# Kernel tuning notes

Measured on AMD Instinct MI355X. Metric: run time of the kernel, lower is better.

Reference implementation:

```python
import jax, jax.numpy as jnp
import numpy as np

H = 1024; NH = 16; HD = H // NH  # hidden, heads, head_dim

def setup_inputs() -> dict:
    key = jax.random.key(0)
    ks = jax.random.split(key, 9)
    s = 1.0 / np.sqrt(H)
    return {
        "hidden_states": jax.random.normal(ks[0], (2, 2048, H), jnp.float32),
        "Wq": jax.random.uniform(ks[1], (H, H), jnp.float32, -s, s),
        "bq": jnp.zeros((H,), jnp.float32),
        "Wk": jax.random.uniform(ks[2], (H, H), jnp.float32, -s, s),
        "bk": jnp.zeros((H,), jnp.float32),
        "Wv": jax.random.uniform(ks[3], (H, H), jnp.float32, -s, s),
        "bv": jnp.zeros((H,), jnp.float32),
        "Wo": jax.random.uniform(ks[4], (H, H), jnp.float32, -s, s),
        "bo": jnp.zeros((H,), jnp.float32),
    }

def reference(hidden_states, Wq, bq, Wk, bk, Wv, bv, Wo, bo):
    B, S, _ = hidden_states.shape
    def heads(x):  # [B,S,H] -> [B,NH,S,HD]
        return x.reshape(B, S, NH, HD).transpose(0, 2, 1, 3)
    q = heads(hidden_states @ Wq + bq)
    k = heads(hidden_states @ Wk + bk)
    v = heads(hidden_states @ Wv + bv)
    scores = jnp.einsum('bhqd,bhkd->bhqk', q, k) / jnp.sqrt(jnp.float32(HD))
    causal = jnp.where(jnp.tril(jnp.ones((S, S), bool)), 0.0, -jnp.inf)
    probs = jax.nn.softmax(scores + causal[None, None], axis=-1)
    ctx = jnp.einsum('bhqk,bhkd->bhqd', probs, v)
    ctx = ctx.transpose(0, 2, 1, 3).reshape(B, S, H)
    return ctx @ Wo + bo
```

## Files before the change

### kernel.cpp

```cpp
#include <hip/hip_runtime.h>
#include <hip/hip_bf16.h>

#define BB 2
#define SS 2048
#define HH 1024
#define NHH 16
#define HDD 64
#define MM (BB*SS)
#define QKV_N (3*HH)

typedef _Float16 f16x8 __attribute__((ext_vector_type(8)));
typedef _Float16 f16x4 __attribute__((ext_vector_type(4)));
typedef float f32x4 __attribute__((ext_vector_type(4)));

#define MFMA16(a,b,c) __builtin_amdgcn_mfma_f32_16x16x32_f16((a),(b),(c),0,0,0)

__device__ __forceinline__ void gl2lds16(const _Float16* g, _Float16* l) {
    __builtin_amdgcn_global_load_lds(
        (const __attribute__((address_space(1))) void*)g,
        (__attribute__((address_space(3))) void*)l, 16, 0, 0);
}

__global__ void prep_kernel(const float* __restrict__ X,
                            const float* __restrict__ W0, const float* __restrict__ W1,
                            const float* __restrict__ W2, const float* __restrict__ W3,
                            _Float16* __restrict__ Xh,
                            _Float16* __restrict__ WqkvT, _Float16* __restrict__ WoT) {
    __shared__ float t[32][33];
    int z = blockIdx.z;
    int tx = threadIdx.x, ty = threadIdx.y;
    if (z >= 4) {
        size_t row0 = (size_t)(z - 4) * 1024 + blockIdx.y * 32;
        int col0 = blockIdx.x * 32;
#pragma unroll
        for (int r = ty; r < 32; r += 8) {
            float v = X[(row0 + r) * HH + col0 + tx];
            Xh[(row0 + r) * HH + col0 + tx] = (_Float16)v;
        }
        return;
    }
    const float* src = (z == 0) ? W0 : (z == 1) ? W1 : (z == 2) ? W2 : W3;
    _Float16* dst = (z < 3) ? (WqkvT + (size_t)z * HH * HH) : WoT;
    int k0 = blockIdx.y * 32, n0 = blockIdx.x * 32;
#pragma unroll
    for (int r = ty; r < 32; r += 8)
        t[r][tx] = src[(size_t)(k0 + r) * HH + (n0 + tx)];
    __syncthreads();
#pragma unroll
    for (int r = ty; r < 32; r += 8)
        dst[(size_t)(n0 + r) * HH + (k0 + tx)] = (_Float16)t[tx][r];
}

template<int MODE>
__global__ __launch_bounds__(256) void gemm128_kernel(
    const _Float16* __restrict__ A, const _Float16* __restrict__ Bt,
    const float* __restrict__ bias0, const float* __restrict__ bias1, const float* __restrict__ bias2,
    _Float16* __restrict__ Qh, _Float16* __restrict__ Kh, _Float16* __restrict__ Vt,
    float* __restrict__ Out)
{
    const int K = HH;
    const int NT = K / 32;
    __shared__ _Float16 smem[16896];

    int row0 = blockIdx.y * 128, n0 = blockIdx.x * 128;
    int tid = threadIdx.x;
    int w = tid >> 6, l = tid & 63, m16 = l & 15, quad = l >> 4;
    int wm = w >> 1, wn = w & 1;

    int srow = w * 32 + (l >> 2);
    int sch = (l & 3) ^ ((l >> 2) & 3) ^ ((l >> 4) & 3);
    const _Float16* aptr = A + (size_t)(row0 + srow) * K + sch * 8;
    const _Float16* bptr = Bt + (size_t)(n0 + srow) * K + sch * 8;

    int gsw = (m16 & 3) ^ ((m16 >> 2) & 3);
    int acol = (quad ^ gsw) * 8;

    f32x4 zero4 = {0.f, 0.f, 0.f, 0.f};
    f32x4 acc[4][4];
#pragma unroll
    for (int i = 0; i < 4; ++i)
#pragma unroll
        for (int j = 0; j < 4; ++j) acc[i][j] = zero4;

    auto stage = [&](int t, int buf) {
        int k0 = t * 32;
        int ao = buf * 4096 + (w * 32) * 32;
        int bo = 8192 + buf * 4096 + (w * 32) * 32;
        gl2lds16(aptr + k0, smem + ao);
        gl2lds16(aptr + (size_t)16 * K + k0, smem + ao + 16 * 32);
        gl2lds16(bptr + k0, smem + bo);
        gl2lds16(bptr + (size_t)16 * K + k0, smem + bo + 16 * 32);
    };

    stage(0, 0);
    for (int t = 0; t < NT; ++t) {
        int cur = t & 1;
        asm volatile("s_waitcnt vmcnt(0)" ::: "memory");
        __syncthreads();
        if (t + 1 < NT) stage(t + 1, cur ^ 1);
        const _Float16* Asr = smem + cur * 4096;
        const _Float16* Bsr = smem + 8192 + cur * 4096;
        f16x8 af[4], bf[4];
#pragma unroll
        for (int i = 0; i < 4; ++i)
            af[i] = *(const f16x8*)&Asr[(wm * 64 + i * 16 + m16) * 32 + acol];
#pragma unroll
        for (int j = 0; j < 4; ++j)
            bf[j] = *(const f16x8*)&Bsr[(wn * 64 + j * 16 + m16) * 32 + acol];
#pragma unroll
        for (int i = 0; i < 4; ++i)
#pragma unroll
            for (int j = 0; j < 4; ++j)
                acc[i][j] = MFMA16(af[i], bf[j], acc[i][j]);
    }

    if (MODE == 1) {
#pragma unroll
        for (int j = 0; j < 4; ++j) {
            int n = n0 + wn * 64 + j * 16 + m16;
            float bi = bias0[n];
#pragma unroll
            for (int i = 0; i < 4; ++i)
#pragma unroll
                for (int r = 0; r < 4; ++r) {
                    int mg = row0 + wm * 64 + i * 16 + quad * 4 + r;
                    Out[(size_t)mg * HH + n] = acc[i][j][r] + bi;
                }
        }
        return;
    }

    int which = n0 >> 10;
    const float* bias = (which == 0) ? bias0 : (which == 1) ? bias1 : bias2;
    __syncthreads();
#pragma unroll
    for (int j = 0; j < 4; ++j) {
        int n_local = wn * 64 + j * 16 + m16;
        float bi = bias[(n0 + n_local) & 1023];
#pragma unroll
        for (int i = 0; i < 4; ++i)
#pragma unroll
            for (int r = 0; r < 4; ++r) {
                int m_local = wm * 64 + i * 16 + quad * 4 + r;
                float v = acc[i][j][r] + bi;
                if (which == 0) v *= 0.18033688011112042f;
                if (which == 2) smem[n_local * 132 + m_local] = (_Float16)v;
                else            smem[m_local * 132 + n_local] = (_Float16)v;
            }
    }
    __syncthreads();

    int b = row0 >> 11, s0 = row0 & 2047;
    if (which == 2) {
#pragma unroll
        for (int p = 0; p < 8; ++p) {
            int n_local = p * 16 + (tid >> 4);
            int schunk = tid & 15;
            f16x8 v = *(const f16x8*)&smem[n_local * 132 + schunk * 8];
            int nw = (n0 + n_local) & 1023;
            int hh = nw >> 6, d = nw & 63;
            *(f16x8*)&Vt[((size_t)(b * NHH + hh) * HDD + d) * SS + s0 + schunk * 8] = v;
        }
    } else {
        _Float16* dst = (which == 0) ? Qh : Kh;
        int hh0 = (n0 & 1023) >> 6;
#pragma unroll
        for (int p = 0; p < 8; ++p) {
            int m_local = p * 16 + (tid >> 4);
            int seg = tid & 15;
            f16x8 v = *(const f16x8*)&smem[m_local * 132 + seg * 8];
            int hh = hh0 + (seg >> 3), d = (seg & 7) * 8;
            *(f16x8*)&dst[((size_t)(b * NHH + hh) * SS + s0 + m_local) * HDD + d] = v;
        }
    }
}

__global__ __launch_bounds__(256, 2) void attn_kernel(
    const _Float16* __restrict__ Qh, const _Float16* __restrict__ Kh,
    const _Float16* __restrict__ Vt, _Float16* __restrict__ Ctx)
{
    __shared__ _Float16 Kb[2][64 * 64];
    __shared__ _Float16 Vb[2][64 * 64];
    __shared__ _Float16 Pl[4][2][16][72];

    int tid = threadIdx.x;
    int w = tid >> 6, l = tid & 63;
    int m16 = l & 15, quad = l >> 4;
    int b = blockIdx.z, h = blockIdx.y;
    int tA = blockIdx.x, tB = 31 - tA;

    const _Float16* Q = Qh + (size_t)(b * NHH + h) * SS * HDD;
    const _Float16* K = Kh + (size_t)(b * NHH + h) * SS * HDD;
    const _Float16* V = Vt + (size_t)(b * NHH + h) * HDD * SS;

    int qbA = tA * 64 + w * 16, qbB = tB * 64 + w * 16;
    f16x8 aqA0 = *(const f16x8*)(Q + (size_t)(qbA + m16) * HDD + quad * 8);
    f16x8 aqA1 = *(const f16x8*)(Q + (size_t)(qbA + m16) * HDD + 32 + quad * 8);
    f16x8 aqB0 = *(const f16x8*)(Q + (size_t)(qbB + m16) * HDD + quad * 8);
    f16x8 aqB1 = *(const f16x8*)(Q + (size_t)(qbB + m16) * HDD + 32 + quad * 8);

    int srow = w * 16 + (l >> 3);
    int sch = (l & 7) ^ (l >> 3);
    const _Float16* kg = K + (size_t)srow * HDD + sch * 8;
    const _Float16* vg = V + (size_t)srow * SS + sch * 8;

    auto stage = [&](int t, int buf) {
        int kt = t * 64;
        gl2lds16(kg + (size_t)kt * HDD, &Kb[buf][(w * 16) * 64]);
        gl2lds16(kg + (size_t)(kt + 8) * HDD, &Kb[buf][(w * 16 + 8) * 64]);
        gl2lds16(vg + kt, &Vb[buf][(w * 16) * 64]);
        gl2lds16(vg + (size_t)8 * SS + kt, &Vb[buf][(w * 16 + 8) * 64]);
    };

    int swz = m16 & 7;
    int cka = (quad ^ swz) * 8;
    int ckb = ((quad + 4) ^ swz) * 8;

    f32x4 zero4 = {0.f, 0.f, 0.f, 0.f};
    f32x4 oA[4], oB[4];
#pragma unroll
    for (int c = 0; c < 4; ++c) { oA[c] = zero4; oB[c] = zero4; }
    float lsA[4] = {0.f, 0.f, 0.f, 0.f}, lsB[4] = {0.f, 0.f, 0.f, 0.f};

    stage(0, 0);
    for (int t = 0; t <= tB; ++t) {
        int cur = t & 1;
        int kt = t * 64;
        bool doA = (t <= tA);
        asm volatile("s_waitcnt vmcnt(0)" ::: "memory");
        __syncthreads();
        if (t + 1 <= tB) stage(t + 1, cur ^ 1);

        f16x8 bk[4][2], bv[4][2];
#pragma unroll
        for (int s = 0; s < 4; ++s) {
            const _Float16* kr = &Kb[cur][(s * 16 + m16) * 64];
            bk[s][0] = *(const f16x8*)(kr + cka);
            bk[s][1] = *(const f16x8*)(kr + ckb);
        }
#pragma unroll
        for (int c = 0; c < 4; ++c) {
            const _Float16* vr = &Vb[cur][(c * 16 + m16) * 64];
            bv[c][0] = *(const f16x8*)(vr + cka);
            bv[c][1] = *(const f16x8*)(vr + ckb);
        }

        f32x4 scB[4], scA[4];
#pragma unroll
        for (int s = 0; s < 4; ++s) {
            scB[s] = MFMA16(aqB0, bk[s][0], zero4);
            scB[s] = MFMA16(aqB1, bk[s][1], scB[s]);
        }
        if (doA) {
#pragma unroll
            for (int s = 0; s < 4; ++s) {
                scA[s] = MFMA16(aqA0, bk[s][0], zero4);
                scA[s] = MFMA16(aqA1, bk[s][1], scA[s]);
            }
        }

#pragma unroll
        for (int s = 0; s < 4; ++s) {
            int key = kt + s * 16 + m16;
#pragma unroll
            for (int r = 0; r < 4; ++r) {
                int qrow = qbB + quad * 4 + r;
                float p = (key > qrow) ? 0.0f : exp2f(scB[s][r]);
                lsB[r] += p;
                Pl[w][0][quad * 4 + r][s * 16 + m16] = (_Float16)p;
            }
        }
        if (doA) {
#pragma unroll
            for (int s = 0; s < 4; ++s) {
                int key = kt + s * 16 + m16;
#pragma unroll
                for (int r = 0; r < 4; ++r) {
                    int qrow = qbA + quad * 4 + r;
                    float p = (key > qrow) ? 0.0f : exp2f(scA[s][r]);
                    lsA[r] += p;
                    Pl[w][1][quad * 4 + r][s * 16 + m16] = (_Float16)p;
                }
            }
        }
        asm volatile("s_waitcnt lgkmcnt(0)" ::: "memory");

        f16x8 pfB0 = *(const f16x8*)&Pl[w][0][m16][quad * 8];
        f16x8 pfB1 = *(const f16x8*)&Pl[w][0][m16][32 + quad * 8];
#pragma unroll
        for (int c = 0; c < 4; ++c) {
            oB[c] = MFMA16(pfB0, bv[c][0], oB[c]);
            oB[c] = MFMA16(pfB1, bv[c][1], oB[c]);
        }
        if (doA) {
            f16x8 pfA0 = *(const f16x8*)&Pl[w][1][m16][quad * 8];
            f16x8 pfA1 = *(const f16x8*)&Pl[w][1][m16][32 + quad * 8];
#pragma unroll
            for (int c = 0; c < 4; ++c) {
                oA[c] = MFMA16(pfA0, bv[c][0], oA[c]);
                oA[c] = MFMA16(pfA1, bv[c][1], oA[c]);
            }
        }
    }

#pragma unroll
    for (int half = 0; half < 2; ++half) {
        f32x4* o = half ? oB : oA;
        float* ls = half ? lsB : lsA;
        int qb = half ? qbB : qbA;
#pragma unroll
        for (int r = 0; r < 4; ++r) {
            float rs = ls[r];
#pragma unroll
            for (int off = 1; off < 16; off <<= 1) rs += __shfl_xor(rs, off);
            float inv = 1.0f / rs;
            size_t rowoff = ((size_t)(b * SS) + qb + quad * 4 + r) * HH + h * HDD;
#pragma unroll
            for (int c = 0; c < 4; ++c)
                Ctx[rowoff + c * 16 + m16] = (_Float16)(o[c][r] * inv);
        }
    }
}

extern "C" void kernel_launch(void* const* d_in, const int* in_sizes, int n_in,
                              void* d_out, int out_size, void* d_ws, size_t ws_size,
                              hipStream_t stream) {
    const float* hs = (const float*)d_in[0];
    const float* Wq = (const float*)d_in[1];
    const float* bq = (const float*)d_in[2];
    const float* Wk = (const float*)d_in[3];
    const float* bk = (const float*)d_in[4];
    const float* Wv = (const float*)d_in[5];
    const float* bv = (const float*)d_in[6];
    const float* Wo = (const float*)d_in[7];
    const float* bo = (const float*)d_in[8];
    float* out = (float*)d_out;

    size_t off = 0;
    auto alloc = [&](size_t bytes) {
        void* p = (char*)d_ws + off;
        off += (bytes + 255) & ~(size_t)255;
        return p;
    };
    _Float16* Xh    = (_Float16*)alloc((size_t)MM * HH * 2);
    _Float16* WqkvT = (_Float16*)alloc((size_t)3 * HH * HH * 2);
    _Float16* WoT   = (_Float16*)alloc((size_t)HH * HH * 2);
    _Float16* Qh    = (_Float16*)alloc((size_t)BB * NHH * SS * HDD * 2);
    _Float16* Kh    = (_Float16*)alloc((size_t)BB * NHH * SS * HDD * 2);
    _Float16* Vt    = (_Float16*)alloc((size_t)BB * NHH * SS * HDD * 2);
    _Float16* Ctx   = (_Float16*)alloc((size_t)MM * HH * 2);

    prep_kernel<<<dim3(32, 32, 8), dim3(32, 8), 0, stream>>>(
        hs, Wq, Wk, Wv, Wo, Xh, WqkvT, WoT);
    gemm128_kernel<0><<<dim3(QKV_N / 128, MM / 128), 256, 0, stream>>>(
        Xh, WqkvT, bq, bk, bv, Qh, Kh, Vt, nullptr);
    attn_kernel<<<dim3(16, NHH, BB), 256, 0, stream>>>(Qh, Kh, Vt, Ctx);
    gemm128_kernel<1><<<dim3(HH / 128, MM / 128), 256, 0, stream>>>(
        Ctx, WoT, bo, bo, bo, nullptr, nullptr, nullptr, out);
}
```

Measured before the change: 206.3 us.

## Triple-buffer GEMM and attention LDS pipelines; vectorize cast and weight transpose

The GEMM and attention kernels move from double to triple buffering of their global-to-LDS tiles, prefetching two tiles ahead. They wait with partial vmcnt counts and a raw s_barrier instead of draining all loads each iteration. Separately, the combined prep kernel is split into a float4 cast kernel for the activations and a 64x64 tiled weight transpose with vectorized loads and f16x8 stores. This costs more LDS per block, which may reduce occupancy, and adds one extra kernel launch.

After: 201.6 us. 2.3% less time.

```diff
diff --git a/kernel.cpp b/kernel.cpp
--- a/kernel.cpp
+++ b/kernel.cpp
@@ -21,34 +21,45 @@
         (__attribute__((address_space(3))) void*)l, 16, 0, 0);
 }
 
-__global__ void prep_kernel(const float* __restrict__ X,
-                            const float* __restrict__ W0, const float* __restrict__ W1,
-                            const float* __restrict__ W2, const float* __restrict__ W3,
-                            _Float16* __restrict__ Xh,
-                            _Float16* __restrict__ WqkvT, _Float16* __restrict__ WoT) {
-    __shared__ float t[32][33];
+__global__ void cast4_kernel(const float* __restrict__ x, _Float16* __restrict__ y, int n4) {
+    int i = blockIdx.x * blockDim.x + threadIdx.x;
+    if (i < n4) {
+        float4 v = ((const float4*)x)[i];
+        f16x4 h = {(_Float16)v.x, (_Float16)v.y, (_Float16)v.z, (_Float16)v.w};
+        ((f16x4*)y)[i] = h;
+    }
+}
+
+__global__ __launch_bounds__(256) void transpose_kernel(
+    const float* __restrict__ W0, const float* __restrict__ W1,
+    const float* __restrict__ W2, const float* __restrict__ W3,
+    _Float16* __restrict__ WqkvT, _Float16* __restrict__ WoT)
+{
+    __shared__ float t[64][65];
     int z = blockIdx.z;
-    int tx = threadIdx.x, ty = threadIdx.y;
-    if (z >= 4) {
-        size_t row0 = (size_t)(z - 4) * 1024 + blockIdx.y * 32;
-        int col0 = blockIdx.x * 32;
-#pragma unroll
-        for (int r = ty; r < 32; r += 8) {
-            float v = X[(row0 + r) * HH + col0 + tx];
-            Xh[(row0 + r) * HH + col0 + tx] = (_Float16)v;
-        }
-        return;
-    }
     const float* src = (z == 0) ? W0 : (z == 1) ? W1 : (z == 2) ? W2 : W3;
     _Float16* dst = (z < 3) ? (WqkvT + (size_t)z * HH * HH) : WoT;
-    int k0 = blockIdx.y * 32, n0 = blockIdx.x * 32;
-#pragma unroll
-    for (int r = ty; r < 32; r += 8)
-        t[r][tx] = src[(size_t)(k0 + r) * HH + (n0 + tx)];
+    int k0 = blockIdx.y * 64, n0 = blockIdx.x * 64;
+    int tid = threadIdx.x;
+
+#pragma unroll
+    for (int p = 0; p < 4; ++p) {
+        int row = p * 16 + (tid >> 4);
+        int col4 = (tid & 15) * 4;
+        float4 v = *(const float4*)&src[(size_t)(k0 + row) * HH + n0 + col4];
+        t[row][col4 + 0] = v.x; t[row][col4 + 1] = v.y;
+        t[row][col4 + 2] = v.z; t[row][col4 + 3] = v.w;
+    }
     __syncthreads();
 #pragma unroll
-    for (int r = ty; r < 32; r += 8)
-        dst[(size_t)(n0 + r) * HH + (k0 + tx)] = (_Float16)t[tx][r];
+    for (int p = 0; p < 2; ++p) {
+        int nc = p * 32 + (tid >> 3);
+        int ch = tid & 7;
+        f16x8 o;
+#pragma unroll
+        for (int j = 0; j < 8; ++j) o[j] = (_Float16)t[ch * 8 + j][nc];
+        *(f16x8*)&dst[(size_t)(n0 + nc) * HH + k0 + ch * 8] = o;
+    }
 }
 
 template<int MODE>
@@ -60,7 +71,7 @@
 {
     const int K = HH;
     const int NT = K / 32;
-    __shared__ _Float16 smem[16896];
+    __shared__ _Float16 smem[24576];
 
     int row0 = blockIdx.y * 128, n0 = blockIdx.x * 128;
     int tid = threadIdx.x;
@@ -82,10 +93,10 @@
 #pragma unroll
         for (int j = 0; j < 4; ++j) acc[i][j] = zero4;
 
-    auto stage = [&](int t, int buf) {
+    auto stage = [&](int t, int s) {
         int k0 = t * 32;
-        int ao = buf * 4096 + (w * 32) * 32;
-        int bo = 8192 + buf * 4096 + (w * 32) * 32;
+        int ao = s * 4096 + (w * 32) * 32;
+        int bo = 12288 + s * 4096 + (w * 32) * 32;
         gl2lds16(aptr + k0, smem + ao);
         gl2lds16(aptr + (size_t)16 * K + k0, smem + ao + 16 * 32);
         gl2lds16(bptr + k0, smem + bo);
@@ -93,13 +104,18 @@
     };
 
     stage(0, 0);
+    stage(1, 1);
+    int cur = 0;
     for (int t = 0; t < NT; ++t) {
-        int cur = t & 1;
-        asm volatile("s_waitcnt vmcnt(0)" ::: "memory");
-        __syncthreads();
-        if (t + 1 < NT) stage(t + 1, cur ^ 1);
+        if (t < NT - 1) asm volatile("s_waitcnt vmcnt(4)" ::: "memory");
+        else            asm volatile("s_waitcnt vmcnt(0)" ::: "memory");
+        asm volatile("s_barrier" ::: "memory");
+        if (t + 2 < NT) {
+            int nxt = cur + 2; if (nxt >= 3) nxt -= 3;
+            stage(t + 2, nxt);
+        }
         const _Float16* Asr = smem + cur * 4096;
-        const _Float16* Bsr = smem + 8192 + cur * 4096;
+        const _Float16* Bsr = smem + 12288 + cur * 4096;
         f16x8 af[4], bf[4];
 #pragma unroll
         for (int i = 0; i < 4; ++i)
@@ -112,6 +128,7 @@
 #pragma unroll
             for (int j = 0; j < 4; ++j)
                 acc[i][j] = MFMA16(af[i], bf[j], acc[i][j]);
+        cur = (cur == 2) ? 0 : cur + 1;
     }
 
     if (MODE == 1) {
@@ -179,8 +196,7 @@
     const _Float16* __restrict__ Qh, const _Float16* __restrict__ Kh,
     const _Float16* __restrict__ Vt, _Float16* __restrict__ Ctx)
 {
-    __shared__ _Float16 Kb[2][64 * 64];
-    __shared__ _Float16 Vb[2][64 * 64];
+    __shared__ _Float16 KV[3 * 8192];
     __shared__ _Float16 Pl[4][2][16][72];
 
     int tid = threadIdx.x;
@@ -204,12 +220,14 @@
     const _Float16* kg = K + (size_t)srow * HDD + sch * 8;
     const _Float16* vg = V + (size_t)srow * SS + sch * 8;
 
-    auto stage = [&](int t, int buf) {
+    auto stage = [&](int t, int s) {
         int kt = t * 64;
-        gl2lds16(kg + (size_t)kt * HDD, &Kb[buf][(w * 16) * 64]);
-        gl2lds16(kg + (size_t)(kt + 8) * HDD, &Kb[buf][(w * 16 + 8) * 64]);
-        gl2lds16(vg + kt, &Vb[buf][(w * 16) * 64]);
-        gl2lds16(vg + (size_t)8 * SS + kt, &Vb[buf][(w * 16 + 8) * 64]);
+        _Float16* kb = &KV[s * 8192];
+        _Float16* vb = &KV[s * 8192 + 4096];
+        gl2lds16(kg + (size_t)kt * HDD, kb + (w * 16) * 64);
+        gl2lds16(kg + (size_t)(kt + 8) * HDD, kb + (w * 16 + 8) * 64);
+        gl2lds16(vg + kt, vb + (w * 16) * 64);
+        gl2lds16(vg + (size_t)8 * SS + kt, vb + (w * 16 + 8) * 64);
     };
 
     int swz = m16 & 7;
@@ -223,24 +241,31 @@
     float lsA[4] = {0.f, 0.f, 0.f, 0.f}, lsB[4] = {0.f, 0.f, 0.f, 0.f};
 
     stage(0, 0);
+    if (1 <= tB) stage(1, 1);
+    int cur = 0;
     for (int t = 0; t <= tB; ++t) {
-        int cur = t & 1;
         int kt = t * 64;
         bool doA = (t <= tA);
-        asm volatile("s_waitcnt vmcnt(0)" ::: "memory");
-        __syncthreads();
-        if (t + 1 <= tB) stage(t + 1, cur ^ 1);
-
+        if (t < tB) asm volatile("s_waitcnt vmcnt(4)" ::: "memory");
+        else        asm volatile("s_waitcnt vmcnt(0)" ::: "memory");
+        asm volatile("s_barrier" ::: "memory");
+        if (t + 2 <= tB) {
+            int nxt = cur + 2; if (nxt >= 3) nxt -= 3;
+            stage(t + 2, nxt);
+        }
+
+        const _Float16* kb = &KV[cur * 8192];
+        const _Float16* vb = &KV[cur * 8192 + 4096];
         f16x8 bk[4][2], bv[4][2];
 #pragma unroll
         for (int s = 0; s < 4; ++s) {
-            const _Float16* kr = &Kb[cur][(s * 16 + m16) * 64];
+            const _Float16* kr = kb + (s * 16 + m16) * 64;
             bk[s][0] = *(const f16x8*)(kr + cka);
             bk[s][1] = *(const f16x8*)(kr + ckb);
         }
 #pragma unroll
         for (int c = 0; c < 4; ++c) {
-            const _Float16* vr = &Vb[cur][(c * 16 + m16) * 64];
+            const _Float16* vr = vb + (c * 16 + m16) * 64;
             bv[c][0] = *(const f16x8*)(vr + cka);
             bv[c][1] = *(const f16x8*)(vr + ckb);
         }
@@ -301,6 +326,7 @@
                 oA[c] = MFMA16(pfA1, bv[c][1], oA[c]);
             }
         }
+        cur = (cur == 2) ? 0 : cur + 1;
     }
 
 #pragma unroll
@@ -350,8 +376,8 @@
     _Float16* Vt    = (_Float16*)alloc((size_t)BB * NHH * SS * HDD * 2);
     _Float16* Ctx   = (_Float16*)alloc((size_t)MM * HH * 2);
 
-    prep_kernel<<<dim3(32, 32, 8), dim3(32, 8), 0, stream>>>(
-        hs, Wq, Wk, Wv, Wo, Xh, WqkvT, WoT);
+    cast4_kernel<<<(MM * HH / 4 + 255) / 256, 256, 0, stream>>>(hs, Xh, MM * HH / 4);
+    transpose_kernel<<<dim3(16, 16, 4), 256, 0, stream>>>(Wq, Wk, Wv, Wo, WqkvT, WoT);
     gemm128_kernel<0><<<dim3(QKV_N / 128, MM / 128), 256, 0, stream>>>(
         Xh, WqkvT, bq, bk, bv, Qh, Kh, Vt, nullptr);
     attn_kernel<<<dim3(16, NHH, BB), 256, 0, stream>>>(Qh, Kh, Vt, Ctx);
```
